# Kernel tuning notes

Hardware: AMD Instinct MI355X
Metric: run time of the kernel (lower is better)

## Reference

```python
import jax, jax.numpy as jnp
import numpy as np

N_NODES = 100000
N_HEDGES = 25000
NNZ = 1600000
IN_CH = 128
HEADS_OUT = 128  # heads * out_channels = 8 * 16


def setup_inputs() -> dict:
    key = jax.random.key(0)
    k1, k2, k3, k4, k5, k6 = jax.random.split(key, 6)
    X = jax.random.normal(k1, (N_NODES, IN_CH), dtype=jnp.float32)
    Wlin = jax.random.normal(k2, (IN_CH, HEADS_OUT), dtype=jnp.float32) * (1.0 / np.sqrt(IN_CH))
    degE = jax.random.uniform(k3, (N_HEDGES, 1), dtype=jnp.float32)
    degV = jax.random.uniform(k4, (N_NODES, 1), dtype=jnp.float32)
    W = jnp.ones((N_HEDGES, 1), dtype=jnp.float32)
    g1_src = jax.random.randint(k5, (NNZ,), 0, N_NODES, dtype=jnp.int32)
    g1_dst = jax.random.randint(k6, (NNZ,), 0, N_HEDGES, dtype=jnp.int32)
    return {"X": X, "Wlin": Wlin, "degE": degE, "degV": degV, "W": W,
            "g1_src": g1_src, "g1_dst": g1_dst}


def reference(X, Wlin, degE, degV, W, g1_src, g1_dst):
    # Linear projection (no bias): [N, in_ch] @ [in_ch, heads*out] -> [N, HO]
    Xp = X @ Wlin
    # Stage 1: copy_u_sum over g1 (node -> hyperedge): out[e] = sum_{v in e} Xp[v]
    Xe = jax.ops.segment_sum(Xp[g1_src], g1_dst, num_segments=N_HEDGES)
    # Elementwise hyperedge scaling: degE then W (W is ones buffer in original)
    Xe = Xe * degE * W
    # Stage 2: copy_u_sum over g2 = g1^T (hyperedge -> node)
    Xv = jax.ops.segment_sum(Xe[g1_dst], g1_src, num_segments=N_NODES)
    # Node degree scaling
    Xv = Xv * degV
    return Xv
```

## Files before the change

kernel.cpp:

```cpp
#include <hip/hip_runtime.h>
#include <hip/hip_bf16.h>


#define CAPE 128
#define CAPV 64
#define LDK  136
#define RW   6250

typedef __attribute__((ext_vector_type(8))) short bf16x8;
typedef __attribute__((ext_vector_type(4))) float f32x4;
typedef __attribute__((ext_vector_type(8))) float f32x8;

__device__ __forceinline__ unsigned short f32_to_bf16(float f) {
    unsigned int u = __float_as_uint(f);
    u += 0x7FFFu + ((u >> 16) & 1u);
    return (unsigned short)(u >> 16);
}
__device__ __forceinline__ float bf16_to_f32(unsigned short h) {
    return __uint_as_float(((unsigned int)h) << 16);
}

__global__ __launch_bounds__(256) void k_init(const float* __restrict__ Wl,
                                              unsigned short* __restrict__ Wt) {
    int idx = blockIdx.x * 256 + threadIdx.x;
    if (idx < 128 * 128) {
        int n = idx >> 7, k = idx & 127;
        Wt[idx] = f32_to_bf16(Wl[k * 128 + n]);
    }
}

__global__ __launch_bounds__(256) void k_gemm(const float* __restrict__ X,
                                              const unsigned short* __restrict__ Wt,
                                              unsigned short* __restrict__ Xp,
                                              int nrows) {
    __shared__ unsigned short XsB[64 * LDK];
    __shared__ unsigned short WtB[128 * LDK];
    const int id  = blockIdx.x;
    const int tid = threadIdx.x;
    const int row0 = id * 64;

    for (int base = tid * 4; base < 64 * 128; base += 1024) {
        int r = base >> 7, c = base & 127;
        float4 v = make_float4(0.f, 0.f, 0.f, 0.f);
        if (row0 + r < nrows) v = *(const float4*)(X + (long)(row0 + r) * 128 + c);
        ushort4 h;
        h.x = f32_to_bf16(v.x); h.y = f32_to_bf16(v.y);
        h.z = f32_to_bf16(v.z); h.w = f32_to_bf16(v.w);
        *(ushort4*)(XsB + r * LDK + c) = h;
    }
    for (int base = tid * 4; base < 128 * 128; base += 1024) {
        int n = base >> 7, k = base & 127;
        ushort4 h = *(const ushort4*)(Wt + base);
        *(ushort4*)(WtB + n * LDK + k) = h;
    }
    __syncthreads();

    const int w    = tid >> 6;
    const int lane = tid & 63;
    const int m    = lane & 15;
    const int quad = lane >> 4;

    f32x4 acc[8];
#pragma unroll
    for (int ct = 0; ct < 8; ++ct) acc[ct] = (f32x4){0.f, 0.f, 0.f, 0.f};

#pragma unroll
    for (int kk = 0; kk < 4; ++kk) {
        bf16x8 a = *(const bf16x8*)(XsB + (w * 16 + m) * LDK + kk * 32 + quad * 8);
#pragma unroll
        for (int ct = 0; ct < 8; ++ct) {
            bf16x8 b = *(const bf16x8*)(WtB + (ct * 16 + m) * LDK + kk * 32 + quad * 8);
            acc[ct] = __builtin_amdgcn_mfma_f32_16x16x32_bf16(a, b, acc[ct], 0, 0, 0);
        }
    }
#pragma unroll
    for (int ct = 0; ct < 8; ++ct) {
#pragma unroll
        for (int r = 0; r < 4; ++r) {
            int row = row0 + w * 16 + quad * 4 + r;
            if (row < nrows)
                Xp[(long)row * 128 + ct * 16 + m] = f32_to_bf16(acc[ct][r]);
        }
    }
}

__global__ __launch_bounds__(256) void k_hist(const int* __restrict__ keyE,
                                              const int* __restrict__ keyV,
                                              int nnz,
                                              unsigned int* __restrict__ histE32,
                                              unsigned int* __restrict__ histV32,
                                              int nE4, int nV4, int che, int chv,
                                              int nchE, int nrE, int nchV, int nrV) {
    __shared__ unsigned int s32[RW];
    int bid = blockIdx.x;
    const int tid = threadIdx.x;
    const int* key; unsigned int* hist; int n4, ch, c, r;
    if (bid < nchE * nrE) {
        key = keyE; hist = histE32; n4 = nE4; ch = che;
        c = bid % nchE; r = bid / nchE;
    } else {
        bid -= nchE * nrE;
        key = keyV; hist = histV32; n4 = nV4; ch = chv;
        c = bid % nchV; r = bid / nchV;
    }
    const int w0 = r * RW;
    const int w1 = (w0 + RW < n4) ? (w0 + RW) : n4;
    const int nw = w1 - w0;
    for (int i = tid; i < nw; i += 256) s32[i] = 0;
    __syncthreads();
    int e0 = c * ch, e1 = e0 + ch; if (e1 > nnz) e1 = nnz;
    for (int e = e0 + tid; e < e1; e += 256) {
        int k = key[e];
        int w = k >> 2;
        if (w >= w0 && w < w1)
            atomicAdd(&s32[w - w0], 1u << ((k & 3) * 8));
    }
    __syncthreads();
    for (int i = tid; i < nw; i += 256)
        hist[(long)c * n4 + w0 + i] = s32[i];
}

__global__ __launch_bounds__(256) void k_scan(unsigned char* __restrict__ histE8,
                                              unsigned char* __restrict__ histV8,
                                              int* __restrict__ cntE,
                                              int* __restrict__ cntV,
                                              int nE, int nV, int nchE, int nchV) {
    int t = blockIdx.x * 256 + threadIdx.x;
    if (t < nE) {
        int b = t, run = 0;
        for (int c = 0; c < nchE; ++c) {
            long a = (long)c * nE + b;
            int h = histE8[a];
            histE8[a] = (unsigned char)run;
            run += h;
        }
        cntE[b] = run;
    } else if (t < nE + nV) {
        int v = t - nE, run = 0;
        for (int c = 0; c < nchV; ++c) {
            long a = (long)c * nV + v;
            int h = histV8[a];
            histV8[a] = (unsigned char)run;
            run += h;
        }
        cntV[v] = run;
    }
}

__global__ __launch_bounds__(256) void k_scatter(const int* __restrict__ src,
                                                 const int* __restrict__ dst,
                                                 int nnz,
                                                 const unsigned char* __restrict__ histE8,
                                                 const unsigned char* __restrict__ histV8,
                                                 int* __restrict__ adjE,
                                                 unsigned short* __restrict__ adjV,
                                                 int nE4, int nV4, int che, int chv,
                                                 int nchE, int nrE, int nchV, int nrV) {
    __shared__ unsigned int c32[RW];
    __shared__ unsigned int sbase[RW];
    int bid = blockIdx.x;
    const int tid = threadIdx.x;
    const bool isE = bid < nchE * nrE;
    const int* key; const int* val; const unsigned int* hist; int n4, ch, c, r;
    if (isE) {
        key = dst; val = src; hist = (const unsigned int*)histE8; n4 = nE4; ch = che;
        c = bid % nchE; r = bid / nchE;
    } else {
        bid -= nchE * nrE;
        key = src; val = dst; hist = (const unsigned int*)histV8; n4 = nV4; ch = chv;
        c = bid % nchV; r = bid / nchV;
    }
    const int w0 = r * RW;
    const int w1 = (w0 + RW < n4) ? (w0 + RW) : n4;
    const int nw = w1 - w0;
    const unsigned int* brow = hist + (long)c * n4 + w0;
    for (int i = tid; i < nw; i += 256) { c32[i] = 0; sbase[i] = brow[i]; }
    __syncthreads();
    int e0 = c * ch, e1 = e0 + ch; if (e1 > nnz) e1 = nnz;
    for (int e = e0 + tid; e < e1; e += 256) {
        int k = key[e];
        int w = k >> 2;
        if (w < w0 || w >= w1) continue;
        int sh = (k & 3) * 8;
        unsigned int old = atomicAdd(&c32[w - w0], 1u << sh);
        int slot = (int)((sbase[w - w0] >> sh) & 0xFF) + (int)((old >> sh) & 0xFF);
        if (isE) {
            if (slot < CAPE) adjE[(long)k * CAPE + slot] = val[e];
        } else {
            if (slot < CAPV) adjV[(long)k * CAPV + slot] = (unsigned short)val[e];
        }
    }
}

__global__ __launch_bounds__(256) void k_gatherE(const unsigned short* __restrict__ Xp,
                                                 const int* __restrict__ cntE,
                                                 const int* __restrict__ adjE,
                                                 const float* __restrict__ degE,
                                                 const float* __restrict__ Wbuf,
                                                 unsigned short* __restrict__ Xe,
                                                 int nE) {
    int t = blockIdx.x * 256 + threadIdx.x;
    int e = t >> 4;
    if (e >= nE) return;
    int c = (t & 15) << 3;
    int len = cntE[e];
    if (len > CAPE) len = CAPE;
    const int* adj = adjE + (long)e * CAPE;
    float acc[8];
#pragma unroll
    for (int q = 0; q < 8; ++q) acc[q] = 0.f;

    int i = 0;
    for (; i + 8 <= len; i += 8) {
        int4 a0 = *(const int4*)(adj + i);
        int4 a1 = *(const int4*)(adj + i + 4);
        int v[8] = {a0.x, a0.y, a0.z, a0.w, a1.x, a1.y, a1.z, a1.w};
        bf16x8 h[8];
#pragma unroll
        for (int j = 0; j < 8; ++j)
            h[j] = *(const bf16x8*)(Xp + (long)v[j] * 128 + c);
#pragma unroll
        for (int j = 0; j < 8; ++j)
#pragma unroll
            for (int q = 0; q < 8; ++q)
                acc[q] += bf16_to_f32((unsigned short)h[j][q]);
    }
    for (; i + 4 <= len; i += 4) {
        int4 a0 = *(const int4*)(adj + i);
        int v[4] = {a0.x, a0.y, a0.z, a0.w};
        bf16x8 h[4];
#pragma unroll
        for (int j = 0; j < 4; ++j)
            h[j] = *(const bf16x8*)(Xp + (long)v[j] * 128 + c);
#pragma unroll
        for (int j = 0; j < 4; ++j)
#pragma unroll
            for (int q = 0; q < 8; ++q)
                acc[q] += bf16_to_f32((unsigned short)h[j][q]);
    }
    for (; i < len; ++i) {
        int v = adj[i];
        bf16x8 h = *(const bf16x8*)(Xp + (long)v * 128 + c);
#pragma unroll
        for (int q = 0; q < 8; ++q)
            acc[q] += bf16_to_f32((unsigned short)h[q]);
    }

    float sc = degE[e] * Wbuf[e];
    bf16x8 o;
#pragma unroll
    for (int q = 0; q < 8; ++q) o[q] = (short)f32_to_bf16(acc[q] * sc);
    *(bf16x8*)(Xe + (long)e * 128 + c) = o;
}

__global__ __launch_bounds__(256) void k_gatherV(const unsigned short* __restrict__ Xe,
                                                 const int* __restrict__ cntV,
                                                 const unsigned short* __restrict__ adjV,
                                                 const float* __restrict__ degV,
                                                 float* __restrict__ out,
                                                 int nV) {
    int t = blockIdx.x * 256 + threadIdx.x;
    int v = t >> 4;
    if (v >= nV) return;
    int c = (t & 15) << 3;
    int len = cntV[v];
    if (len > CAPV) len = CAPV;
    const unsigned short* adj = adjV + (long)v * CAPV;
    float acc[8];
#pragma unroll
    for (int q = 0; q < 8; ++q) acc[q] = 0.f;

    int i = 0;
    for (; i + 8 <= len; i += 8) {
        ushort4 a0 = *(const ushort4*)(adj + i);
        ushort4 a1 = *(const ushort4*)(adj + i + 4);
        int e[8] = {a0.x, a0.y, a0.z, a0.w, a1.x, a1.y, a1.z, a1.w};
        bf16x8 h[8];
#pragma unroll
        for (int j = 0; j < 8; ++j)
            h[j] = *(const bf16x8*)(Xe + (long)e[j] * 128 + c);
#pragma unroll
        for (int j = 0; j < 8; ++j)
#pragma unroll
            for (int q = 0; q < 8; ++q)
                acc[q] += bf16_to_f32((unsigned short)h[j][q]);
    }
    for (; i + 4 <= len; i += 4) {
        ushort4 a0 = *(const ushort4*)(adj + i);
        int e[4] = {a0.x, a0.y, a0.z, a0.w};
        bf16x8 h[4];
#pragma unroll
        for (int j = 0; j < 4; ++j)
            h[j] = *(const bf16x8*)(Xe + (long)e[j] * 128 + c);
#pragma unroll
        for (int j = 0; j < 4; ++j)
#pragma unroll
            for (int q = 0; q < 8; ++q)
                acc[q] += bf16_to_f32((unsigned short)h[j][q]);
    }
    for (; i < len; ++i) {
        int e = adj[i];
        bf16x8 h = *(const bf16x8*)(Xe + (long)e * 128 + c);
#pragma unroll
        for (int q = 0; q < 8; ++q)
            acc[q] += bf16_to_f32((unsigned short)h[q]);
    }

    float sc = degV[v];
    f32x8 o;
#pragma unroll
    for (int q = 0; q < 8; ++q) o[q] = acc[q] * sc;
    *(f32x8*)(out + (long)v * 128 + c) = o;
}

__global__ __launch_bounds__(256) void zero_f4(float4* __restrict__ p, int n4) {
    int i = blockIdx.x * 256 + threadIdx.x;
    if (i < n4) p[i] = make_float4(0.f, 0.f, 0.f, 0.f);
}

__global__ __launch_bounds__(256) void gemm_xw_f32(const float* __restrict__ X,
                                                   const float* __restrict__ Wl,
                                                   float* __restrict__ Xp,
                                                   int nrows) {
    __shared__ float Xs[32 * 128];
    const int tid = threadIdx.x;
    const int row0 = blockIdx.x * 32;
    for (int i = tid * 4; i < 32 * 128; i += 256 * 4) {
        int r = row0 + (i >> 7);
        float4 v = make_float4(0.f, 0.f, 0.f, 0.f);
        if (r < nrows) v = *(const float4*)(X + (long)row0 * 128 + i);
        *(float4*)(Xs + i) = v;
    }
    __syncthreads();
    const int col = tid & 127;
    const int rg  = (tid >> 7) * 16;
    float acc[16];
#pragma unroll
    for (int r = 0; r < 16; ++r) acc[r] = 0.f;
    for (int k = 0; k < 128; k += 4) {
        const float w0 = Wl[(k + 0) * 128 + col];
        const float w1 = Wl[(k + 1) * 128 + col];
        const float w2 = Wl[(k + 2) * 128 + col];
        const float w3 = Wl[(k + 3) * 128 + col];
#pragma unroll
        for (int r = 0; r < 16; ++r) {
            float4 x = *(const float4*)(Xs + (rg + r) * 128 + k);
            acc[r] = fmaf(x.w, w3, fmaf(x.z, w2, fmaf(x.y, w1, fmaf(x.x, w0, acc[r]))));
        }
    }
#pragma unroll
    for (int r = 0; r < 16; ++r) {
        int row = row0 + rg + r;
        if (row < nrows) Xp[(long)row * 128 + col] = acc[r];
    }
}

__global__ __launch_bounds__(256) void scatter_to_hedges(const float* __restrict__ Xp,
                                                         const int* __restrict__ src,
                                                         const int* __restrict__ dst,
                                                         float* __restrict__ Xe,
                                                         int nnz) {
    int t = blockIdx.x * 256 + threadIdx.x;
    int e = t >> 5;
    if (e >= nnz) return;
    int c = (t & 31) << 2;
    int s = src[e], d = dst[e];
    float4 v = *(const float4*)(Xp + (long)s * 128 + c);
    float* o = Xe + (long)d * 128 + c;
    atomicAdd(o + 0, v.x); atomicAdd(o + 1, v.y);
    atomicAdd(o + 2, v.z); atomicAdd(o + 3, v.w);
}

__global__ __launch_bounds__(256) void scatter_to_nodes(const float* __restrict__ Xe,
                                                        const int* __restrict__ src,
                                                        const int* __restrict__ dst,
                                                        const float* __restrict__ degE,
                                                        const float* __restrict__ Wbuf,
                                                        const float* __restrict__ degV,
                                                        float* __restrict__ out,
                                                        int nnz) {
    int t = blockIdx.x * 256 + threadIdx.x;
    int e = t >> 5;
    if (e >= nnz) return;
    int c = (t & 31) << 2;
    int s = src[e], d = dst[e];
    float sc = degE[d] * Wbuf[d] * degV[s];
    float4 v = *(const float4*)(Xe + (long)d * 128 + c);
    float* o = out + (long)s * 128 + c;
    atomicAdd(o + 0, v.x * sc); atomicAdd(o + 1, v.y * sc);
    atomicAdd(o + 2, v.z * sc); atomicAdd(o + 3, v.w * sc);
}

extern "C" void kernel_launch(void* const* d_in, const int* in_sizes, int n_in,
                              void* d_out, int out_size, void* d_ws, size_t ws_size,
                              hipStream_t stream) {
    const float* X    = (const float*)d_in[0];
    const float* Wlin = (const float*)d_in[1];
    const float* degE = (const float*)d_in[2];
    const float* degV = (const float*)d_in[3];
    const float* Wbuf = (const float*)d_in[4];
    const int* g1_src = (const int*)d_in[5];
    const int* g1_dst = (const int*)d_in[6];

    const int nE  = in_sizes[2];
    const int nV  = in_sizes[3];
    const int nnz = in_sizes[5];

    float* out = (float*)d_out;
    char* ws = (char*)d_ws;

    auto layout_size = [&](int cE, int cV) -> size_t {
        size_t o = 0;
        o += (size_t)nE * CAPE * 4;
        o += (size_t)nV * CAPV * 2;
        o += (size_t)nE * 4 + (size_t)nV * 4;
        o += (size_t)cE * nE;
        size_t hv = (size_t)cV * nV;
        size_t xe = (size_t)nE * 128 * 2;
        o += (hv > xe) ? hv : xe;
        o += 128 * 128 * 2;
        o += 4096;
        return o;
    };

    int nchE = 64, nchV = 64;
    if (layout_size(nchE, nchV) > ws_size) { nchE = 32; nchV = 32; }

    const bool aligned4 = ((nE & 3) == 0) && ((nV & 3) == 0);

    if (aligned4 && layout_size(nchE, nchV) <= ws_size) {
        size_t boff = 0;
        auto alloc = [&](size_t bytes) -> char* {
            char* p = ws + boff;
            boff += (bytes + 255) & ~(size_t)255;
            return p;
        };
        int* adjE            = (int*)alloc((size_t)nE * CAPE * 4);
        unsigned short* adjV = (unsigned short*)alloc((size_t)nV * CAPV * 2);
        int* cntE            = (int*)alloc((size_t)nE * 4);
        int* cntV            = (int*)alloc((size_t)nV * 4);
        unsigned char* histE8 = (unsigned char*)alloc((size_t)nchE * nE);
        size_t hv = (size_t)nchV * nV;
        size_t xe = (size_t)nE * 128 * 2;
        char* region          = alloc((hv > xe) ? hv : xe);
        unsigned char* histV8 = (unsigned char*)region;
        unsigned short* Xe    = (unsigned short*)region;
        unsigned short* Wt    = (unsigned short*)alloc((size_t)128 * 128 * 2);

        unsigned short* Xp_bf = (unsigned short*)d_out;

        const int nE4 = nE >> 2, nV4 = nV >> 2;
        const int nrE = (nE4 + RW - 1) / RW;
        const int nrV = (nV4 + RW - 1) / RW;
        const int che = (nnz + nchE - 1) / nchE;
        const int chv = (nnz + nchV - 1) / nchV;

        k_init<<<64, 256, 0, stream>>>(Wlin, Wt);

        int nGemm = (nV + 63) / 64;
        k_gemm<<<nGemm, 256, 0, stream>>>(X, Wt, Xp_bf, nV);

        k_hist<<<nchE * nrE + nchV * nrV, 256, 0, stream>>>(
            g1_dst, g1_src, nnz,
            (unsigned int*)histE8, (unsigned int*)histV8,
            nE4, nV4, che, chv, nchE, nrE, nchV, nrV);

        k_scan<<<(nE + nV + 255) / 256, 256, 0, stream>>>(histE8, histV8,
                                                          cntE, cntV,
                                                          nE, nV, nchE, nchV);

        k_scatter<<<nchE * nrE + nchV * nrV, 256, 0, stream>>>(
            g1_src, g1_dst, nnz, histE8, histV8, adjE, adjV,
            nE4, nV4, che, chv, nchE, nrE, nchV, nrV);

        int gE = (nE * 16 + 255) / 256;
        k_gatherE<<<gE, 256, 0, stream>>>(Xp_bf, cntE, adjE, degE, Wbuf, Xe, nE);

        int gV = (nV * 16 + 255) / 256;
        k_gatherV<<<gV, 256, 0, stream>>>(Xe, cntV, adjV, degV, out, nV);
    } else {
        float* XeF = (float*)d_ws;
        float* Xp  = out;
        int n4 = nE * 128 / 4;
        zero_f4<<<(n4 + 255) / 256, 256, 0, stream>>>((float4*)XeF, n4);
        gemm_xw_f32<<<(nV + 31) / 32, 256, 0, stream>>>(X, Wlin, Xp, nV);
        long th = (long)nnz * 32;
        scatter_to_hedges<<<(int)((th + 255) / 256), 256, 0, stream>>>(Xp, g1_src, g1_dst,
                                                                       XeF, nnz);
        int m4 = out_size / 4;
        zero_f4<<<(m4 + 255) / 256, 256, 0, stream>>>((float4*)out, m4);
        scatter_to_nodes<<<(int)((th + 255) / 256), 256, 0, stream>>>(XeF, g1_src, g1_dst,
                                                                      degE, Wbuf, degV,
                                                                      out, nnz);
    }
}
```

Measured before the change: 382.1 us.

## Fuse GEMM and histogram kernels into one launch and raise chunk counts

Result: slower. 424.7 us (+11.1%).

```diff
diff --git a/kernel.cpp b/kernel.cpp
--- a/kernel.cpp
+++ b/kernel.cpp
@@ -29,71 +29,71 @@
     }
 }
 
-__global__ __launch_bounds__(256) void k_gemm(const float* __restrict__ X,
-                                              const unsigned short* __restrict__ Wt,
-                                              unsigned short* __restrict__ Xp,
-                                              int nrows) {
-    __shared__ unsigned short XsB[64 * LDK];
-    __shared__ unsigned short WtB[128 * LDK];
-    const int id  = blockIdx.x;
-    const int tid = threadIdx.x;
-    const int row0 = id * 64;
-
-    for (int base = tid * 4; base < 64 * 128; base += 1024) {
-        int r = base >> 7, c = base & 127;
-        float4 v = make_float4(0.f, 0.f, 0.f, 0.f);
-        if (row0 + r < nrows) v = *(const float4*)(X + (long)(row0 + r) * 128 + c);
-        ushort4 h;
-        h.x = f32_to_bf16(v.x); h.y = f32_to_bf16(v.y);
-        h.z = f32_to_bf16(v.z); h.w = f32_to_bf16(v.w);
-        *(ushort4*)(XsB + r * LDK + c) = h;
-    }
-    for (int base = tid * 4; base < 128 * 128; base += 1024) {
-        int n = base >> 7, k = base & 127;
-        ushort4 h = *(const ushort4*)(Wt + base);
-        *(ushort4*)(WtB + n * LDK + k) = h;
-    }
-    __syncthreads();
-
-    const int w    = tid >> 6;
-    const int lane = tid & 63;
-    const int m    = lane & 15;
-    const int quad = lane >> 4;
-
-    f32x4 acc[8];
-#pragma unroll
-    for (int ct = 0; ct < 8; ++ct) acc[ct] = (f32x4){0.f, 0.f, 0.f, 0.f};
-
-#pragma unroll
-    for (int kk = 0; kk < 4; ++kk) {
-        bf16x8 a = *(const bf16x8*)(XsB + (w * 16 + m) * LDK + kk * 32 + quad * 8);
-#pragma unroll
-        for (int ct = 0; ct < 8; ++ct) {
-            bf16x8 b = *(const bf16x8*)(WtB + (ct * 16 + m) * LDK + kk * 32 + quad * 8);
-            acc[ct] = __builtin_amdgcn_mfma_f32_16x16x32_bf16(a, b, acc[ct], 0, 0, 0);
-        }
-    }
-#pragma unroll
-    for (int ct = 0; ct < 8; ++ct) {
-#pragma unroll
-        for (int r = 0; r < 4; ++r) {
-            int row = row0 + w * 16 + quad * 4 + r;
-            if (row < nrows)
-                Xp[(long)row * 128 + ct * 16 + m] = f32_to_bf16(acc[ct][r]);
-        }
-    }
-}
-
-__global__ __launch_bounds__(256) void k_hist(const int* __restrict__ keyE,
-                                              const int* __restrict__ keyV,
-                                              int nnz,
-                                              unsigned int* __restrict__ histE32,
-                                              unsigned int* __restrict__ histV32,
-                                              int nE4, int nV4, int che, int chv,
-                                              int nchE, int nrE, int nchV, int nrV) {
-    __shared__ unsigned int s32[RW];
+__global__ __launch_bounds__(256) void k_gemm_hist(
+    const float* __restrict__ X, const unsigned short* __restrict__ Wt,
+    unsigned short* __restrict__ Xp, int nrows, int nGemm,
+    const int* __restrict__ keyE, const int* __restrict__ keyV, int nnz,
+    unsigned int* __restrict__ histE32, unsigned int* __restrict__ histV32,
+    int nE4, int nV4, int che, int chv,
+    int nchE, int nrE, int nchV, int nrV)
+{
+    __shared__ union {
+        struct { unsigned short Xs[64 * LDK]; unsigned short Wt[128 * LDK]; } g;
+        unsigned int s32[RW];
+    } sm;
+
     int bid = blockIdx.x;
     const int tid = threadIdx.x;
+
+    if (bid < nGemm) {
+        const int row0 = bid * 64;
+        for (int base = tid * 4; base < 64 * 128; base += 1024) {
+            int r = base >> 7, c = base & 127;
+            float4 v = make_float4(0.f, 0.f, 0.f, 0.f);
+            if (row0 + r < nrows) v = *(const float4*)(X + (long)(row0 + r) * 128 + c);
+            ushort4 h;
+            h.x = f32_to_bf16(v.x); h.y = f32_to_bf16(v.y);
+            h.z = f32_to_bf16(v.z); h.w = f32_to_bf16(v.w);
+            *(ushort4*)(sm.g.Xs + r * LDK + c) = h;
+        }
+        for (int base = tid * 4; base < 128 * 128; base += 1024) {
+            int n = base >> 7, k = base & 127;
+            ushort4 h = *(const ushort4*)(Wt + base);
+            *(ushort4*)(sm.g.Wt + n * LDK + k) = h;
+        }
+        __syncthreads();
+
+        const int w    = tid >> 6;
+        const int lane = tid & 63;
+        const int m    = lane & 15;
+        const int quad = lane >> 4;
+
+        f32x4 acc[8];
+#pragma unroll
+        for (int ct = 0; ct < 8; ++ct) acc[ct] = (f32x4){0.f, 0.f, 0.f, 0.f};
+
+#pragma unroll
+        for (int kk = 0; kk < 4; ++kk) {
+            bf16x8 a = *(const bf16x8*)(sm.g.Xs + (w * 16 + m) * LDK + kk * 32 + quad * 8);
+#pragma unroll
+            for (int ct = 0; ct < 8; ++ct) {
+                bf16x8 b = *(const bf16x8*)(sm.g.Wt + (ct * 16 + m) * LDK + kk * 32 + quad * 8);
+                acc[ct] = __builtin_amdgcn_mfma_f32_16x16x32_bf16(a, b, acc[ct], 0, 0, 0);
+            }
+        }
+#pragma unroll
+        for (int ct = 0; ct < 8; ++ct) {
+#pragma unroll
+            for (int r = 0; r < 4; ++r) {
+                int row = row0 + w * 16 + quad * 4 + r;
+                if (row < nrows)
+                    Xp[(long)row * 128 + ct * 16 + m] = f32_to_bf16(acc[ct][r]);
+            }
+        }
+        return;
+    }
+
+    bid -= nGemm;
     const int* key; unsigned int* hist; int n4, ch, c, r;
     if (bid < nchE * nrE) {
         key = keyE; hist = histE32; n4 = nE4; ch = che;
@@ -106,18 +106,18 @@
     const int w0 = r * RW;
     const int w1 = (w0 + RW < n4) ? (w0 + RW) : n4;
     const int nw = w1 - w0;
-    for (int i = tid; i < nw; i += 256) s32[i] = 0;
+    for (int i = tid; i < nw; i += 256) sm.s32[i] = 0;
     __syncthreads();
     int e0 = c * ch, e1 = e0 + ch; if (e1 > nnz) e1 = nnz;
     for (int e = e0 + tid; e < e1; e += 256) {
         int k = key[e];
         int w = k >> 2;
         if (w >= w0 && w < w1)
-            atomicAdd(&s32[w - w0], 1u << ((k & 3) * 8));
+            atomicAdd(&sm.s32[w - w0], 1u << ((k & 3) * 8));
     }
     __syncthreads();
     for (int i = tid; i < nw; i += 256)
-        hist[(long)c * n4 + w0 + i] = s32[i];
+        hist[(long)c * n4 + w0 + i] = sm.s32[i];
 }
 
 __global__ __launch_bounds__(256) void k_scan(unsigned char* __restrict__ histE8,
@@ -423,8 +423,10 @@
         return o;
     };
 
-    int nchE = 64, nchV = 64;
-    if (layout_size(nchE, nchV) > ws_size) { nchE = 32; nchV = 32; }
+    int nchE = 256, nchV = 256;
+    if (layout_size(nchE, nchV) > ws_size) { nchE = 256; nchV = 128; }
+    if (layout_size(nchE, nchV) > ws_size) { nchE = 128; nchV = 128; }
+    if (layout_size(nchE, nchV) > ws_size) { nchE = 64;  nchV = 64;  }
 
     const bool aligned4 = ((nE & 3) == 0) && ((nV & 3) == 0);
 
@@ -458,9 +460,9 @@
         k_init<<<64, 256, 0, stream>>>(Wlin, Wt);
 
         int nGemm = (nV + 63) / 64;
-        k_gemm<<<nGemm, 256, 0, stream>>>(X, Wt, Xp_bf, nV);
-
-        k_hist<<<nchE * nrE + nchV * nrV, 256, 0, stream>>>(
+        int gHist = nchE * nrE + nchV * nrV;
+        k_gemm_hist<<<nGemm + gHist, 256, 0, stream>>>(
+            X, Wt, Xp_bf, nV, nGemm,
             g1_dst, g1_src, nnz,
             (unsigned int*)histE8, (unsigned int*)histV8,
             nE4, nV4, che, chv, nchE, nrE, nchV, nrV);
@@ -469,7 +471,7 @@
                                                           cntE, cntV,
                                                           nE, nV, nchE, nchV);
 
-        k_scatter<<<nchE * nrE + nchV * nrV, 256, 0, stream>>>(
+        k_scatter<<<gHist, 256, 0, stream>>>(
             g1_src, g1_dst, nnz, histE8, histV8, adjE, adjV,
             nE4, nV4, che, chv, nchE, nrE, nchV, nrV);
 
```
